# Optimization experiments

Measured on AMD Instinct MI355X. Metric: run time of the kernel, lower is better.

The kernel has to match this reference:

```python
import jax, jax.numpy as jnp
import numpy as np

# Architecture constants (from init_kwargs)
B, L, D = 4, 2048, 512          # docs, tokens per doc, embed_dim
H = 8                           # num_heads -> head_dim 64
HALF_WIN = (33 - 1) // 2        # window_size=33 -> 16 keys each side
GAP = 1 + 1                     # dilation_gap=1 -> step 2
OVERLAP = HALF_WIN * GAP        # 32
W = 2 * HALF_WIN                # 32 keys per token (self excluded)


def setup_inputs() -> dict:
    key = jax.random.key(0)
    ks = jax.random.split(key, 5)
    s = 0.02
    return {
        "begin": jax.random.normal(ks[0], (B, OVERLAP, D), dtype=jnp.float32),
        "main": jax.random.normal(ks[1], (B, L, D), dtype=jnp.float32),
        "end": jax.random.normal(ks[2], (B, OVERLAP, D), dtype=jnp.float32),
        "in_proj_w": jax.random.normal(ks[3], (3 * D, D), dtype=jnp.float32) * s,
        "in_proj_b": jnp.zeros((3 * D,), dtype=jnp.float32),
        "out_proj_w": jax.random.normal(ks[4], (D, D), dtype=jnp.float32) * s,
        "out_proj_b": jnp.zeros((D,), dtype=jnp.float32),
    }


def reference(begin, main, end, in_proj_w, in_proj_b, out_proj_w, out_proj_b):
    hd = D // H
    # padded[b, overlap + t] == main[b, t]; begin/end provide halo context.
    padded = jnp.concatenate([begin, main, end], axis=1)  # [B, L+2*OVERLAP, D]

    # Static dilated-window gather indices (matches the shifted-cat loops).
    offsets = np.concatenate(
        [np.arange(-OVERLAP, 0, GAP), np.arange(GAP, OVERLAP + GAP, GAP)]
    )  # [W]
    idx = np.arange(L)[:, None] + offsets[None, :] + OVERLAP  # [L, W]

    wq, wk, wv = jnp.split(in_proj_w, 3, axis=0)   # each [D, D]
    bq, bk, bv = jnp.split(in_proj_b, 3, axis=0)

    q = main @ wq.T + bq                            # [B, L, D]
    k_full = padded @ wk.T + bk                     # project once, then gather
    v_full = padded @ wv.T + bv
    k = k_full[:, idx]                              # [B, L, W, D]
    v = v_full[:, idx]                              # [B, L, W, D]

    qh = q.reshape(B, L, H, hd)
    kh = k.reshape(B, L, W, H, hd)
    vh = v.reshape(B, L, W, H, hd)

    scores = jnp.einsum('blhd,blwhd->blhw', qh, kh) / jnp.sqrt(jnp.float32(hd))
    attn = jax.nn.softmax(scores, axis=-1)          # [B, L, H, W]
    o = jnp.einsum('blhw,blwhd->blhd', attn, vh).reshape(B, L, D)
    o = o @ out_proj_w.T + out_proj_b               # [B, L, D]

    # cat(main, attn_out) per token, then concat docs along dim 0.
    return jnp.concatenate([main, o], axis=-1).reshape(B * L, 2 * D)
```

## Files before the change

### kernel.cpp

```cpp
#include <hip/hip_runtime.h>

typedef unsigned short u16;
typedef unsigned int u32;
typedef __attribute__((ext_vector_type(8))) __bf16 bf16x8;
typedef __attribute__((ext_vector_type(4))) float f32x4;

#define NB 4
#define SEQ 2048
#define DIM 512
#define NH 8
#define HD 64
#define OV 32
#define PD 2112

__device__ __forceinline__ u16 f2bf(float f) {
  union { float f; u32 u; } x; x.f = f;
  u32 r = x.u + 0x7fffu + ((x.u >> 16) & 1u);
  return (u16)(r >> 16);
}


__global__ void k_pack_padded(const float* __restrict__ begin,
                              const float* __restrict__ mainp,
                              const float* __restrict__ endp,
                              u16* __restrict__ pad) {
  int i = blockIdx.x * 256 + threadIdx.x;
  if (i >= NB * PD * (DIM / 4)) return;
  int d4 = (i & 127) * 4;
  int p = (i >> 7) % PD;
  int b = i / (PD * (DIM / 4));
  const float* src;
  if (p < OV)            src = begin + ((size_t)(b * OV + p)) * DIM + d4;
  else if (p < OV + SEQ) src = mainp + ((size_t)(b * SEQ + (p - OV))) * DIM + d4;
  else                   src = endp + ((size_t)(b * OV + (p - OV - SEQ))) * DIM + d4;
  float4 v = *(const float4*)src;
  u32 lo = (u32)f2bf(v.x) | ((u32)f2bf(v.y) << 16);
  u32 hi = (u32)f2bf(v.z) | ((u32)f2bf(v.w) << 16);
  *(uint2*)&pad[(size_t)i * 4] = make_uint2(lo, hi);
}

__global__ void k_f32_to_bf16(const float* __restrict__ src, u16* __restrict__ dst, int n4) {
  int i = blockIdx.x * 256 + threadIdx.x;
  if (i >= n4) return;
  float4 v = *(const float4*)&src[(size_t)i * 4];
  u32 lo = (u32)f2bf(v.x) | ((u32)f2bf(v.y) << 16);
  u32 hi = (u32)f2bf(v.z) | ((u32)f2bf(v.w) << 16);
  *(uint2*)&dst[(size_t)i * 4] = make_uint2(lo, hi);
}


__device__ __forceinline__ void gemm_tile_128(const u16* __restrict__ A,
                                              const u16* __restrict__ Bw,
                                              int tm0, int tn0,
                                              u16 As[128][40], u16 Bs[128][40],
                                              f32x4 acc[4][4]) {
  const int tid = threadIdx.x;
  const int lane = tid & 63;
  const int wv = tid >> 6;
  const int wm = (wv >> 1) * 64, wn = (wv & 1) * 64;
  const int r0 = tid >> 2;
  const int sg = (tid & 3) * 8;
  const int rr = lane & 15;
  const int kk = (lane >> 4) * 8;
  for (int k0 = 0; k0 < 512; k0 += 32) {
    {
      int r1 = r0, r2 = r0 + 64;
      *(uint4*)&As[r1][sg] = *(const uint4*)&A[(size_t)(tm0 + r1) * 512 + k0 + sg];
      *(uint4*)&As[r2][sg] = *(const uint4*)&A[(size_t)(tm0 + r2) * 512 + k0 + sg];
      *(uint4*)&Bs[r1][sg] = *(const uint4*)&Bw[(size_t)(tn0 + r1) * 512 + k0 + sg];
      *(uint4*)&Bs[r2][sg] = *(const uint4*)&Bw[(size_t)(tn0 + r2) * 512 + k0 + sg];
    }
    __syncthreads();
    bf16x8 af[4], bfr[4];
#pragma unroll
    for (int f = 0; f < 4; ++f) {
      af[f] = *(const bf16x8*)&As[wm + f * 16 + rr][kk];
      bfr[f] = *(const bf16x8*)&Bs[wn + f * 16 + rr][kk];
    }
#pragma unroll
    for (int fm = 0; fm < 4; ++fm)
#pragma unroll
      for (int fn = 0; fn < 4; ++fn)
        acc[fm][fn] = __builtin_amdgcn_mfma_f32_16x16x32_bf16(af[fm], bfr[fn], acc[fm][fn], 0, 0, 0);
    __syncthreads();
  }
}

__global__ __launch_bounds__(256) void k_gemm_qkv(const u16* __restrict__ A,
                                                  const u16* __restrict__ Bw,
                                                  const float* __restrict__ bias,
                                                  u16* __restrict__ qh,
                                                  u16* __restrict__ kh,
                                                  u16* __restrict__ vt) {
  __shared__ __align__(16) u16 As[128][40];
  __shared__ __align__(16) u16 Bs[128][40];
  int bx = blockIdx.x;
  int tm0 = (bx / 12) * 128, tn0 = (bx % 12) * 128;
  f32x4 acc[4][4] = {};
  gemm_tile_128(A, Bw, tm0, tn0, As, Bs, acc);
  int lane = threadIdx.x & 63, wv = threadIdx.x >> 6;
  int wm = (wv >> 1) * 64, wn = (wv & 1) * 64;
#pragma unroll
  for (int fm = 0; fm < 4; ++fm)
#pragma unroll
    for (int fn = 0; fn < 4; ++fn) {
      int gcol = tn0 + wn + fn * 16 + (lane & 15);
      int reg = gcol >> 9, c = gcol & 511, h = c >> 6, d = c & 63;
      float bb = bias[gcol];
      int grow0 = tm0 + wm + fm * 16 + (lane >> 4) * 4;
      int b = grow0 / PD, p0 = grow0 - b * PD;
      if (reg == 2) {
        u16 u0 = f2bf(acc[fm][fn][0] + bb);
        u16 u1 = f2bf(acc[fm][fn][1] + bb);
        u16 u2 = f2bf(acc[fm][fn][2] + bb);
        u16 u3 = f2bf(acc[fm][fn][3] + bb);
        *(uint2*)&vt[(((size_t)(b * NH + h)) * HD + d) * PD + p0] =
            make_uint2((u32)u0 | ((u32)u1 << 16), (u32)u2 | ((u32)u3 << 16));
      } else if (reg == 1) {
#pragma unroll
        for (int r = 0; r < 4; ++r)
          kh[(((size_t)(b * NH + h)) * PD + p0 + r) * HD + d] = f2bf(acc[fm][fn][r] + bb);
      } else {
#pragma unroll
        for (int r = 0; r < 4; ++r) {
          int p = p0 + r;
          if (p >= OV && p < OV + SEQ)
            qh[(((size_t)(b * NH + h)) * SEQ + (p - OV)) * HD + d] = f2bf(acc[fm][fn][r] + bb);
        }
      }
    }
}

__global__ __launch_bounds__(256) void k_gemm_oproj(const u16* __restrict__ A,
                                                    const u16* __restrict__ Bw,
                                                    const float* __restrict__ bias,
                                                    float* __restrict__ out) {
  __shared__ __align__(16) u16 As[128][40];
  __shared__ __align__(16) u16 Bs[128][40];
  int bx = blockIdx.x;
  int tm0 = (bx / 4) * 128, tn0 = (bx % 4) * 128;
  f32x4 acc[4][4] = {};
  gemm_tile_128(A, Bw, tm0, tn0, As, Bs, acc);
  int lane = threadIdx.x & 63, wv = threadIdx.x >> 6;
  int wm = (wv >> 1) * 64, wn = (wv & 1) * 64;
#pragma unroll
  for (int fm = 0; fm < 4; ++fm)
#pragma unroll
    for (int fn = 0; fn < 4; ++fn) {
      int j = tn0 + wn + fn * 16 + (lane & 15);
      float bb = bias[j];
#pragma unroll
      for (int r = 0; r < 4; ++r) {
        int row = tm0 + wm + fm * 16 + (lane >> 4) * 4 + r;
        out[(size_t)row * 1024 + 512 + j] = acc[fm][fn][r] + bb;
      }
    }
}


__device__ __forceinline__ int pswz(int slot, int key) {
  return (slot < 8) ? (slot ^ (key & 7)) : ((slot & 12) | ((slot ^ (key & 3)) & 3));
}

__global__ __launch_bounds__(256) void k_attn(const u16* __restrict__ qh,
                                              const u16* __restrict__ kh,
                                              const u16* __restrict__ vt,
                                              u16* __restrict__ ob) {
  __shared__ __align__(16) u16 Ks[128 * 64];
  __shared__ __align__(16) u16 Vs[64 * 128];
  __shared__ __align__(16) u16 Qs[64 * 64];
  __shared__ __align__(16) u16 Ps[4 * 16 * 96];
  const int tid = threadIdx.x;
  const int lane = tid & 63;
  const int wq = tid >> 6;
  const int g = lane >> 4, qi = lane & 15;
  const int bx = blockIdx.x;
  const int tile = bx & 31, h = (bx >> 5) & 7, b = bx >> 8;
  const int l0 = tile * 64;
  const size_t bh = (size_t)(b * NH + h);

  {
    const u16* kg = kh + (bh * PD + l0) * HD;
#pragma unroll
    for (int i = 0; i < 4; ++i) {
      int c = tid + 256 * i;
      int row = c >> 3, slot = c & 7;
      *(uint4*)&Ks[row * 64 + ((slot ^ (row & 7)) << 3)] =
          *(const uint4*)&kg[(size_t)row * HD + slot * 8];
    }
    const u16* vg = vt + bh * HD * PD + l0;
#pragma unroll
    for (int i = 0; i < 4; ++i) {
      int c = tid + 256 * i;
      int d = c >> 4, slot = c & 15;
      *(uint4*)&Vs[d * 128 + ((slot ^ (d & 15)) << 3)] =
          *(const uint4*)&vg[(size_t)d * PD + slot * 8];
    }
    const u16* qg = qh + (bh * SEQ + l0) * HD;
#pragma unroll
    for (int i = 0; i < 2; ++i) {
      int c = tid + 256 * i;
      int row = c >> 3, slot = c & 7;
      *(uint4*)&Qs[row * 64 + ((slot ^ (row & 7)) << 3)] =
          *(const uint4*)&qg[(size_t)row * HD + slot * 8];
    }
  }
  __syncthreads();

  bf16x8 bq[2];
  {
    int qrow = 16 * wq + qi;
#pragma unroll
    for (int ks = 0; ks < 2; ++ks)
      bq[ks] = *(const bf16x8*)&Qs[qrow * 64 + ((((g + 4 * ks)) ^ (qrow & 7)) << 3)];
  }
  f32x4 sa[5];
#pragma unroll
  for (int tt = 0; tt < 5; ++tt) { f32x4 z = {0.f, 0.f, 0.f, 0.f}; sa[tt] = z; }
#pragma unroll
  for (int tt = 0; tt < 5; ++tt) {
    int krow = 16 * (wq + tt) + qi;
#pragma unroll
    for (int ks = 0; ks < 2; ++ks) {
      bf16x8 ak = *(const bf16x8*)&Ks[krow * 64 + (((g + 4 * ks) ^ (krow & 7)) << 3)];
      sa[tt] = __builtin_amdgcn_mfma_f32_16x16x32_bf16(ak, bq[ks], sa[tt], 0, 0, 0);
    }
  }

  float m = -1e30f;
#pragma unroll
  for (int tt = 0; tt < 5; ++tt)
#pragma unroll
    for (int r = 0; r < 4; ++r) {
      int rel = 16 * tt + 4 * g + r - qi;
      bool val = (rel >= 0) && (rel <= 64) && (rel != 32) && ((rel & 1) == 0);
      if (val) m = fmaxf(m, sa[tt][r]);
    }
  m = fmaxf(m, __shfl_xor(m, 16));
  m = fmaxf(m, __shfl_xor(m, 32));
  float p[5][4];
  float sum = 0.f;
#pragma unroll
  for (int tt = 0; tt < 5; ++tt)
#pragma unroll
    for (int r = 0; r < 4; ++r) {
      int rel = 16 * tt + 4 * g + r - qi;
      bool val = (rel >= 0) && (rel <= 64) && (rel != 32) && ((rel & 1) == 0);
      p[tt][r] = val ? __expf((sa[tt][r] - m) * 0.125f) : 0.f;
      sum += p[tt][r];
    }
  sum += __shfl_xor(sum, 16);
  sum += __shfl_xor(sum, 32);
  float inv = 1.f / sum;

  {
    int prow = 16 * wq + qi;
    int colb = (wq & 1) << 4;
#pragma unroll
    for (int tt = 0; tt < 5; ++tt) {
#pragma unroll
      for (int pp = 0; pp < 2; ++pp) {
        int e = 4 * g + 2 * pp;
        int slot = ((colb + 16 * tt) >> 3) + (e >> 3);
        int swz = pswz(slot, qi);
        u32 w = (u32)f2bf(p[tt][2 * pp] * inv) | ((u32)f2bf(p[tt][2 * pp + 1] * inv) << 16);
        *(u32*)&Ps[prow * 96 + swz * 8 + (e & 7)] = w;
      }
    }
    int zslot = ((wq & 1) ? 0 : 10) + ((lane >> 4) & 1);
    int half = lane >> 5;
    int swz = pswz(zslot, qi);
    uint2 z2 = make_uint2(0u, 0u);
    *(uint2*)&Ps[(16 * wq + qi) * 96 + swz * 8 + half * 4] = z2;
  }
  __syncthreads();

  f32x4 oa[4];
#pragma unroll
  for (int dt = 0; dt < 4; ++dt) { f32x4 z = {0.f, 0.f, 0.f, 0.f}; oa[dt] = z; }
  int kbo = (wq >= 2) ? 1 : 0;
#pragma unroll
  for (int kt = 0; kt < 3; ++kt) {
    int slot = 4 * kt + g;
    int swz = pswz(slot, qi);
    bf16x8 pa = *(const bf16x8*)&Ps[(16 * wq + qi) * 96 + swz * 8];
    int sabs = 4 * (kt + kbo) + g;
#pragma unroll
    for (int dt = 0; dt < 4; ++dt) {
      int d = 16 * dt + qi;
      bf16x8 bv = *(const bf16x8*)&Vs[d * 128 + ((sabs ^ (d & 15)) << 3)];
      oa[dt] = __builtin_amdgcn_mfma_f32_16x16x32_bf16(pa, bv, oa[dt], 0, 0, 0);
    }
  }

  u16* og = ob + ((size_t)b * SEQ + l0 + 16 * wq) * DIM + h * HD;
#pragma unroll
  for (int dt = 0; dt < 4; ++dt)
#pragma unroll
    for (int r = 0; r < 4; ++r) {
      int qo = 4 * g + r;
      og[(size_t)qo * DIM + 16 * dt + qi] = f2bf(oa[dt][r]);
    }
}

__global__ void k_copy_main(const float* __restrict__ mainp, float* __restrict__ out) {
  int i = blockIdx.x * 256 + threadIdx.x;
  if (i >= SEQ * NB * (DIM / 4)) return;
  int row = i >> 7;
  int c4 = (i & 127) * 4;
  *(float4*)&out[(size_t)row * 1024 + c4] = *(const float4*)&mainp[(size_t)i * 4];
}

extern "C" void kernel_launch(void* const* d_in, const int* in_sizes, int n_in,
                              void* d_out, int out_size, void* d_ws, size_t ws_size,
                              hipStream_t stream) {
  const float* begin = (const float*)d_in[0];
  const float* mainp = (const float*)d_in[1];
  const float* endp = (const float*)d_in[2];
  const float* w_in_f = (const float*)d_in[3];
  const float* b_in = (const float*)d_in[4];
  const float* w_out_f = (const float*)d_in[5];
  const float* b_out = (const float*)d_in[6];
  float* out = (float*)d_out;

  char* ws = (char*)d_ws;
  u16* pad_bf = (u16*)ws; ws += (size_t)NB * PD * DIM * 2;
  u16* w_in = (u16*)ws;   ws += (size_t)3 * DIM * DIM * 2;
  u16* w_out = (u16*)ws;  ws += (size_t)DIM * DIM * 2;
  u16* qhb = (u16*)ws;    ws += (size_t)NB * NH * SEQ * HD * 2;
  u16* khb = (u16*)ws;    ws += (size_t)NB * NH * PD * HD * 2;
  u16* vtb = (u16*)ws;    ws += (size_t)NB * NH * HD * PD * 2;
  u16* ob = (u16*)ws;     ws += (size_t)NB * SEQ * DIM * 2;

  k_pack_padded<<<(NB * PD * (DIM / 4) + 255) / 256, 256, 0, stream>>>(begin, mainp, endp, pad_bf);
  k_f32_to_bf16<<<(3 * DIM * DIM / 4 + 255) / 256, 256, 0, stream>>>(w_in_f, w_in, 3 * DIM * DIM / 4);
  k_f32_to_bf16<<<(DIM * DIM / 4 + 255) / 256, 256, 0, stream>>>(w_out_f, w_out, DIM * DIM / 4);
  k_gemm_qkv<<<66 * 12, 256, 0, stream>>>(pad_bf, w_in, b_in, qhb, khb, vtb);
  k_attn<<<NB * NH * (SEQ / 64), 256, 0, stream>>>(qhb, khb, vtb, ob);
  k_gemm_oproj<<<64 * 4, 256, 0, stream>>>(ob, w_out, b_out, out);
  k_copy_main<<<(SEQ * NB * (DIM / 4) + 255) / 256, 256, 0, stream>>>(mainp, out);
}
```

Measured before the change: 83.05 us.

## Merge prep kernels, double-buffer GEMM via global_load_lds, fuse main copy into oproj

Combines the padded-input pack and the two weight conversions into one launch, and folds the main-tensor copy into the output-projection GEMM, removing three kernel launches. The shared GEMM loop now uses direct global-to-LDS loads into double-buffered, unpadded tiles, prefetching the next K slice while MFMAs run on the current one, and drops one barrier per iteration. Removing the LDS row padding may add bank conflicts on fragment reads, and the copy inside the oproj GEMM adds memory traffic to that kernel.

```diff
diff --git a/kernel.cpp b/kernel.cpp
--- a/kernel.cpp
+++ b/kernel.cpp
@@ -13,76 +13,102 @@
 #define OV 32
 #define PD 2112
 
+#define PACK_N (NB * PD * (DIM / 4))
+#define WIN_N (3 * DIM * DIM / 4)
+#define WOUT_N (DIM * DIM / 4)
+
+#define GLL(g, l)                                                  \
+  __builtin_amdgcn_global_load_lds(                                \
+      (const __attribute__((address_space(1))) void*)(g),          \
+      (__attribute__((address_space(3))) void*)(l), 16, 0, 0)
+
 __device__ __forceinline__ u16 f2bf(float f) {
   union { float f; u32 u; } x; x.f = f;
   u32 r = x.u + 0x7fffu + ((x.u >> 16) & 1u);
   return (u16)(r >> 16);
 }
 
-
-__global__ void k_pack_padded(const float* __restrict__ begin,
-                              const float* __restrict__ mainp,
-                              const float* __restrict__ endp,
-                              u16* __restrict__ pad) {
+__global__ void k_prep(const float* __restrict__ begin,
+                       const float* __restrict__ mainp,
+                       const float* __restrict__ endp,
+                       const float* __restrict__ w_in_f,
+                       const float* __restrict__ w_out_f,
+                       u16* __restrict__ pad,
+                       u16* __restrict__ w_in,
+                       u16* __restrict__ w_out) {
   int i = blockIdx.x * 256 + threadIdx.x;
-  if (i >= NB * PD * (DIM / 4)) return;
-  int d4 = (i & 127) * 4;
-  int p = (i >> 7) % PD;
-  int b = i / (PD * (DIM / 4));
   const float* src;
-  if (p < OV)            src = begin + ((size_t)(b * OV + p)) * DIM + d4;
-  else if (p < OV + SEQ) src = mainp + ((size_t)(b * SEQ + (p - OV))) * DIM + d4;
-  else                   src = endp + ((size_t)(b * OV + (p - OV - SEQ))) * DIM + d4;
+  u16* dst;
+  if (i < PACK_N) {
+    int d4 = (i & 127) * 4;
+    int p = (i >> 7) % PD;
+    int b = i / (PD * (DIM / 4));
+    if (p < OV)            src = begin + ((size_t)(b * OV + p)) * DIM + d4;
+    else if (p < OV + SEQ) src = mainp + ((size_t)(b * SEQ + (p - OV))) * DIM + d4;
+    else                   src = endp + ((size_t)(b * OV + (p - OV - SEQ))) * DIM + d4;
+    dst = pad + (size_t)i * 4;
+  } else if (i < PACK_N + WIN_N) {
+    int j = i - PACK_N;
+    src = w_in_f + (size_t)j * 4;
+    dst = w_in + (size_t)j * 4;
+  } else if (i < PACK_N + WIN_N + WOUT_N) {
+    int j = i - PACK_N - WIN_N;
+    src = w_out_f + (size_t)j * 4;
+    dst = w_out + (size_t)j * 4;
+  } else {
+    return;
+  }
   float4 v = *(const float4*)src;
   u32 lo = (u32)f2bf(v.x) | ((u32)f2bf(v.y) << 16);
   u32 hi = (u32)f2bf(v.z) | ((u32)f2bf(v.w) << 16);
-  *(uint2*)&pad[(size_t)i * 4] = make_uint2(lo, hi);
-}
-
-__global__ void k_f32_to_bf16(const float* __restrict__ src, u16* __restrict__ dst, int n4) {
-  int i = blockIdx.x * 256 + threadIdx.x;
-  if (i >= n4) return;
-  float4 v = *(const float4*)&src[(size_t)i * 4];
-  u32 lo = (u32)f2bf(v.x) | ((u32)f2bf(v.y) << 16);
-  u32 hi = (u32)f2bf(v.z) | ((u32)f2bf(v.w) << 16);
-  *(uint2*)&dst[(size_t)i * 4] = make_uint2(lo, hi);
-}
-
-
-__device__ __forceinline__ void gemm_tile_128(const u16* __restrict__ A,
-                                              const u16* __restrict__ Bw,
-                                              int tm0, int tn0,
-                                              u16 As[128][40], u16 Bs[128][40],
-                                              f32x4 acc[4][4]) {
+  *(uint2*)dst = make_uint2(lo, hi);
+}
+
+
+__device__ __forceinline__ void gemm_loop(const u16* __restrict__ A,
+                                          const u16* __restrict__ Bw,
+                                          int tm0, int tn0,
+                                          u16* As, u16* Bs,
+                                          f32x4 acc[4][4]) {
   const int tid = threadIdx.x;
   const int lane = tid & 63;
-  const int wv = tid >> 6;
-  const int wm = (wv >> 1) * 64, wn = (wv & 1) * 64;
-  const int r0 = tid >> 2;
-  const int sg = (tid & 3) * 8;
+  const int w = tid >> 6;
   const int rr = lane & 15;
-  const int kk = (lane >> 4) * 8;
-  for (int k0 = 0; k0 < 512; k0 += 32) {
-    {
-      int r1 = r0, r2 = r0 + 64;
-      *(uint4*)&As[r1][sg] = *(const uint4*)&A[(size_t)(tm0 + r1) * 512 + k0 + sg];
-      *(uint4*)&As[r2][sg] = *(const uint4*)&A[(size_t)(tm0 + r2) * 512 + k0 + sg];
-      *(uint4*)&Bs[r1][sg] = *(const uint4*)&Bw[(size_t)(tn0 + r1) * 512 + k0 + sg];
-      *(uint4*)&Bs[r2][sg] = *(const uint4*)&Bw[(size_t)(tn0 + r2) * 512 + k0 + sg];
-    }
-    __syncthreads();
+  const int kb = (lane >> 4) * 8;
+  const int wm = (w >> 1) * 64, wn = (w & 1) * 64;
+  const u16* gA = A + (size_t)(tm0 + w * 32 + (lane >> 2)) * 512 + (lane & 3) * 8;
+  const u16* gB = Bw + (size_t)(tn0 + w * 32 + (lane >> 2)) * 512 + (lane & 3) * 8;
+  char* lA = (char*)As + w * 2048;
+  char* lB = (char*)Bs + w * 2048;
+
+  GLL(gA, lA); GLL(gA + 16 * 512, lA + 1024);
+  GLL(gB, lB); GLL(gB + 16 * 512, lB + 1024);
+  __syncthreads();
+
+#pragma unroll
+  for (int t = 0; t < 16; ++t) {
+    const int cur = t & 1;
+    if (t < 15) {
+      const int nxt = cur ^ 1;
+      const u16* ga = gA + (t + 1) * 32;
+      const u16* gb = gB + (t + 1) * 32;
+      GLL(ga, lA + nxt * 8192); GLL(ga + 16 * 512, lA + nxt * 8192 + 1024);
+      GLL(gb, lB + nxt * 8192); GLL(gb + 16 * 512, lB + nxt * 8192 + 1024);
+    }
+    const u16* cA = As + cur * 4096;
+    const u16* cB = Bs + cur * 4096;
     bf16x8 af[4], bfr[4];
 #pragma unroll
     for (int f = 0; f < 4; ++f) {
-      af[f] = *(const bf16x8*)&As[wm + f * 16 + rr][kk];
-      bfr[f] = *(const bf16x8*)&Bs[wn + f * 16 + rr][kk];
+      af[f] = *(const bf16x8*)&cA[(wm + f * 16 + rr) * 32 + kb];
+      bfr[f] = *(const bf16x8*)&cB[(wn + f * 16 + rr) * 32 + kb];
     }
 #pragma unroll
     for (int fm = 0; fm < 4; ++fm)
 #pragma unroll
       for (int fn = 0; fn < 4; ++fn)
         acc[fm][fn] = __builtin_amdgcn_mfma_f32_16x16x32_bf16(af[fm], bfr[fn], acc[fm][fn], 0, 0, 0);
-    __syncthreads();
+    if (t < 15) __syncthreads();
   }
 }
 
@@ -92,12 +118,12 @@
                                                   u16* __restrict__ qh,
                                                   u16* __restrict__ kh,
                                                   u16* __restrict__ vt) {
-  __shared__ __align__(16) u16 As[128][40];
-  __shared__ __align__(16) u16 Bs[128][40];
+  __shared__ __align__(16) u16 As[2][128][32];
+  __shared__ __align__(16) u16 Bs[2][128][32];
   int bx = blockIdx.x;
   int tm0 = (bx / 12) * 128, tn0 = (bx % 12) * 128;
   f32x4 acc[4][4] = {};
-  gemm_tile_128(A, Bw, tm0, tn0, As, Bs, acc);
+  gemm_loop(A, Bw, tm0, tn0, &As[0][0][0], &Bs[0][0][0], acc);
   int lane = threadIdx.x & 63, wv = threadIdx.x >> 6;
   int wm = (wv >> 1) * 64, wn = (wv & 1) * 64;
 #pragma unroll
@@ -134,13 +160,19 @@
 __global__ __launch_bounds__(256) void k_gemm_oproj(const u16* __restrict__ A,
                                                     const u16* __restrict__ Bw,
                                                     const float* __restrict__ bias,
+                                                    const float* __restrict__ mainp,
                                                     float* __restrict__ out) {
-  __shared__ __align__(16) u16 As[128][40];
-  __shared__ __align__(16) u16 Bs[128][40];
+  __shared__ __align__(16) u16 As[2][128][32];
+  __shared__ __align__(16) u16 Bs[2][128][32];
   int bx = blockIdx.x;
-  int tm0 = (bx / 4) * 128, tn0 = (bx % 4) * 128;
+  int tm0 = (bx >> 2) * 128, tn0 = (bx & 3) * 128;
+  for (int i = threadIdx.x; i < 4096; i += 256) {
+    int r = i >> 5, c4 = (i & 31) * 4;
+    *(float4*)&out[(size_t)(tm0 + r) * 1024 + tn0 + c4] =
+        *(const float4*)&mainp[(size_t)(tm0 + r) * 512 + tn0 + c4];
+  }
   f32x4 acc[4][4] = {};
-  gemm_tile_128(A, Bw, tm0, tn0, As, Bs, acc);
+  gemm_loop(A, Bw, tm0, tn0, &As[0][0][0], &Bs[0][0][0], acc);
   int lane = threadIdx.x & 63, wv = threadIdx.x >> 6;
   int wm = (wv >> 1) * 64, wn = (wv & 1) * 64;
 #pragma unroll
@@ -156,7 +188,6 @@
       }
     }
 }
-
 
 __device__ __forceinline__ int pswz(int slot, int key) {
   return (slot < 8) ? (slot ^ (key & 7)) : ((slot & 12) | ((slot ^ (key & 3)) & 3));
@@ -303,14 +334,6 @@
     }
 }
 
-__global__ void k_copy_main(const float* __restrict__ mainp, float* __restrict__ out) {
-  int i = blockIdx.x * 256 + threadIdx.x;
-  if (i >= SEQ * NB * (DIM / 4)) return;
-  int row = i >> 7;
-  int c4 = (i & 127) * 4;
-  *(float4*)&out[(size_t)row * 1024 + c4] = *(const float4*)&mainp[(size_t)i * 4];
-}
-
 extern "C" void kernel_launch(void* const* d_in, const int* in_sizes, int n_in,
                               void* d_out, int out_size, void* d_ws, size_t ws_size,
                               hipStream_t stream) {
@@ -332,11 +355,9 @@
   u16* vtb = (u16*)ws;    ws += (size_t)NB * NH * HD * PD * 2;
   u16* ob = (u16*)ws;     ws += (size_t)NB * SEQ * DIM * 2;
 
-  k_pack_padded<<<(NB * PD * (DIM / 4) + 255) / 256, 256, 0, stream>>>(begin, mainp, endp, pad_bf);
-  k_f32_to_bf16<<<(3 * DIM * DIM / 4 + 255) / 256, 256, 0, stream>>>(w_in_f, w_in, 3 * DIM * DIM / 4);
-  k_f32_to_bf16<<<(DIM * DIM / 4 + 255) / 256, 256, 0, stream>>>(w_out_f, w_out, DIM * DIM / 4);
+  k_prep<<<(PACK_N + WIN_N + WOUT_N + 255) / 256, 256, 0, stream>>>(
+      begin, mainp, endp, w_in_f, w_out_f, pad_bf, w_in, w_out);
   k_gemm_qkv<<<66 * 12, 256, 0, stream>>>(pad_bf, w_in, b_in, qhb, khb, vtb);
   k_attn<<<NB * NH * (SEQ / 64), 256, 0, stream>>>(qhb, khb, vtb, ob);
-  k_gemm_oproj<<<64 * 4, 256, 0, stream>>>(ob, w_out, b_out, out);
-  k_copy_main<<<(SEQ * NB * (DIM / 4) + 255) / 256, 256, 0, stream>>>(mainp, out);
-}
+  k_gemm_oproj<<<64 * 4, 256, 0, stream>>>(ob, w_out, b_out, mainp, out);
+}
```

New measurement: 77.64 us. -6.5%, faster.
